# Optimization experiments

Hardware: AMD Instinct MI355X
Metric: run time of the kernel (lower is better)

The kernel has to match this reference:

```python
import jax, jax.numpy as jnp
import numpy as np

E, T, H, I, K = 16, 2048, 1024, 512, 2  # experts, tokens, hidden, intermediate, top_k


def setup_inputs() -> dict:
    key = jax.random.key(0)
    k1, k2, k3, k4, k5 = jax.random.split(key, 5)
    hidden_states = jax.random.normal(k1, (T, H), dtype=jnp.float32)
    topk_weights = jax.random.uniform(k2, (T, K), dtype=jnp.float32)
    topk_indices = jax.random.randint(k3, (T, K), 0, E, dtype=jnp.int32)
    # learned expert params, viewed per expert as in _view_experts_weight()
    gate_up_proj = jax.random.normal(k4, (E, H, 2 * I), dtype=jnp.float32) * 0.02
    down_proj = jax.random.normal(k5, (E, I, H), dtype=jnp.float32) * 0.02
    return {
        "hidden_states": hidden_states,
        "topk_weights": topk_weights,
        "topk_indices": topk_indices,
        "gate_up_proj": gate_up_proj,
        "down_proj": down_proj,
    }


def reference(hidden_states, topk_weights, topk_indices, gate_up_proj, down_proj):
    """MoE experts: per-expert gate_up GEMM -> silu-gate -> down GEMM,
    combined with top-k routing weights (index_add over tokens in the original).

    Equivalent dense formulation: combine[e, t] = sum_k topk_weights[t, k] * [topk_indices[t, k] == e];
    out = sum_e expert_e(hidden_states) * combine[e][:, None]. Tokens not routed to e get
    weight 0, matching the original gather/scatter-add exactly (including duplicate
    expert ids within a token, which accumulate).
    """
    num_experts = gate_up_proj.shape[0]
    one_hot = jax.nn.one_hot(topk_indices, num_experts, dtype=topk_weights.dtype)  # [T, K, E]
    combine = jnp.einsum("tk,tke->et", topk_weights, one_hot)  # [E, T]

    def body(acc, xs):
        w_gu, w_d, w = xs  # [H, 2I], [I, H], [T]
        gate_up = hidden_states @ w_gu  # [T, 2I]
        gate, up = jnp.split(gate_up, 2, axis=-1)
        expert_out = (jax.nn.silu(gate) * up) @ w_d  # [T, H]
        return acc + expert_out * w[:, None], None

    init = jnp.zeros_like(hidden_states)
    out, _ = jax.lax.scan(body, init, (gate_up_proj, down_proj, combine))
    return out.astype(hidden_states.dtype)
```

## Files before the change

kernel.cpp:

```cpp
#include <hip/hip_runtime.h>

#define E_ 16
#define T_ 2048
#define H_ 1024
#define I_ 512
#define NPAIR 4096
#define BM 128
#define MAXTILE 48

typedef __bf16 bf16x8 __attribute__((ext_vector_type(8)));
typedef float  f32x4  __attribute__((ext_vector_type(4)));

static __device__ __forceinline__ unsigned short f2bf(float f) {
    __bf16 h = (__bf16)f;
    return __builtin_bit_cast(unsigned short, h);
}

static __device__ __forceinline__ uint4 pack8(const float* v) {
    union { unsigned short us[8]; uint4 u; } r;
    #pragma unroll
    for (int i = 0; i < 8; ++i) r.us[i] = f2bf(v[i]);
    return r.u;
}

static __device__ __forceinline__ void gl_lds16(const void* g, void* l) {
    __builtin_amdgcn_global_load_lds(
        (const __attribute__((address_space(1))) unsigned int*)g,
        (__attribute__((address_space(3))) unsigned int*)l,
        16, 0, 0);
}

__global__ __launch_bounds__(256) void route_kernel(
    const float* __restrict__ tw, const int* __restrict__ ti,
    int* __restrict__ offs, int* __restrict__ tile_e, int* __restrict__ tile_r,
    int* __restrict__ pair_ts, float* __restrict__ pair_w)
{
    __shared__ unsigned short hist[256][E_];
    __shared__ int ebase[E_];
    const int tid = threadIdx.x;

    int e_loc[16];
    unsigned short h[E_];
    for (int e = 0; e < E_; ++e) h[e] = 0;
    for (int i = 0; i < 16; ++i) {
        int p = tid * 16 + i;
        int e = ti[p];
        e_loc[i] = e;
        h[e]++;
    }
    for (int e = 0; e < E_; ++e) hist[tid][e] = h[e];
    __syncthreads();

    if (tid < E_) {
        int e = tid, run = 0;
        for (int t = 0; t < 256; ++t) {
            unsigned short c = hist[t][e];
            hist[t][e] = (unsigned short)run;
            run += c;
        }
        ebase[e] = run;
    }
    __syncthreads();
    if (tid == 0) {
        int run = 0, nt = 0;
        for (int e = 0; e < E_; ++e) {
            int c = ebase[e];
            offs[e] = run; ebase[e] = run;
            for (int r = 0; r < c; r += BM) { tile_e[nt] = e; tile_r[nt] = r; ++nt; }
            run += c;
        }
        offs[E_] = run;
        for (; nt < MAXTILE; ++nt) tile_e[nt] = -1;
    }
    __syncthreads();

    int cur[E_];
    for (int e = 0; e < E_; ++e) cur[e] = ebase[e] + hist[tid][e];
    for (int i = 0; i < 16; ++i) {
        int p = tid * 16 + i;
        int e = e_loc[i];
        int pos = cur[e]++;
        pair_ts[pos] = p;
        pair_w[pos]  = tw[p];
    }
}

__global__ __launch_bounds__(256) void gather_kernel(
    const float* __restrict__ X, const int* __restrict__ pair_ts,
    unsigned short* __restrict__ Ag)
{
    const int q = blockIdx.x;
    const int t = pair_ts[q] >> 1;
    const int c = threadIdx.x * 4;
    const float4 x = *(const float4*)&X[(size_t)t * H_ + c];
    ushort4 b; b.x = f2bf(x.x); b.y = f2bf(x.y); b.z = f2bf(x.z); b.w = f2bf(x.w);
    *(ushort4*)&Ag[(size_t)q * H_ + c] = b;
}

#define MFMA_TILE(AS, BS)                                                              \
    _Pragma("unroll")                                                                  \
    for (int kkj = 0; kkj < 2; ++kkj) {                                                \
        const int j0 = kkj * 4;                                                        \
        bf16x8 af[4], bfr[2];                                                          \
        _Pragma("unroll")                                                              \
        for (int m = 0; m < 4; ++m)                                                    \
            af[m] = *(const bf16x8*)&AS[wm * 64 + m * 16 + lrow][((j0 + lk) ^ (lrow & 7)) * 8]; \
        _Pragma("unroll")                                                              \
        for (int n = 0; n < 2; ++n)                                                    \
            bfr[n] = *(const bf16x8*)&BS[wn * 32 + n * 16 + lrow][((j0 + lk) ^ (lrow & 7)) * 8]; \
        _Pragma("unroll")                                                              \
        for (int m = 0; m < 4; ++m)                                                    \
            _Pragma("unroll")                                                          \
            for (int n = 0; n < 2; ++n)                                                \
                acc[m][n] = __builtin_amdgcn_mfma_f32_16x16x32_bf16(af[m], bfr[n], acc[m][n], 0, 0, 0); \
    }

#define PIPE_STEP(KT, NT, BSTRIDE, ASC, ASN, BSC, BSN, BVC, BVN)                       \
    {                                                                                  \
        if ((KT) + 1 < (NT)) {                                                         \
            const int kb_ = ((KT) + 1) * 64;                                           \
            _Pragma("unroll")                                                          \
            for (int i = 0; i < 4; ++i) gl_lds16(asrc[i] + kb_, &ASN[w * 32 + i * 8][0]); \
            *(uint4*)&BSN[bn][bg0] = pack8(&BVC[0]);                                   \
            *(uint4*)&BSN[bn][bg1] = pack8(&BVC[8]);                                   \
        }                                                                              \
        if ((KT) + 2 < (NT)) {                                                         \
            const int kb2_ = ((KT) + 2) * 64;                                          \
            _Pragma("unroll")                                                          \
            for (int i = 0; i < 16; ++i)                                               \
                BVN[i] = bsrc[(size_t)(kb2_ + w * 16 + i) * (BSTRIDE)];                \
        }                                                                              \
        MFMA_TILE(ASC, BSC)                                                            \
        __syncthreads();                                                               \
    }

__global__ __launch_bounds__(256, 3) void gemm1_kernel(
    const unsigned short* __restrict__ Ag, const float* __restrict__ W1,
    const int* __restrict__ offs, const int* __restrict__ tile_e,
    const int* __restrict__ tile_r, unsigned short* __restrict__ act)
{
    const int e = tile_e[blockIdx.y];
    if (e < 0) return;
    const int rbeg = offs[e], rend = offs[e + 1];
    const int ne   = rend - rbeg;
    const int row0 = tile_r[blockIdx.y];
    const int c0 = blockIdx.x * 32;

    __shared__ unsigned short As0[128][64], As1[128][64];
    __shared__ unsigned short Bs0[64][64],  Bs1[64][64];

    const int tid  = threadIdx.x;
    const int lane = tid & 63;
    const int w    = tid >> 6;
    const int wm   = w >> 1, wn = w & 1;
    const int lrow = lane & 15;
    const int lk   = lane >> 4;

    const float* __restrict__ W1e = W1 + (size_t)e * (H_ * 2 * I_);

    const int r8 = lane >> 3, gr = lane & 7;
    const unsigned short* asrc[4];
    #pragma unroll
    for (int i = 0; i < 4; ++i) {
        int q = rbeg + row0 + w * 32 + i * 8 + r8;
        if (q > rend - 1) q = rend - 1;
        asrc[i] = Ag + (size_t)q * H_ + (gr ^ r8) * 8;
    }

    const int bn   = lane;
    const int bcol = ((bn >> 4) & 1) * I_ + c0 + (bn >> 5) * 16 + (bn & 15);
    const float* __restrict__ bsrc = W1e + bcol;
    const int bg0 = ((2 * w)     ^ (bn & 7)) * 8;
    const int bg1 = ((2 * w + 1) ^ (bn & 7)) * 8;

    f32x4 acc[4][2];
    #pragma unroll
    for (int m = 0; m < 4; ++m)
        #pragma unroll
        for (int n = 0; n < 2; ++n)
            acc[m][n] = f32x4{0.f, 0.f, 0.f, 0.f};

    float bv0[16], bv1[16];
    #pragma unroll
    for (int i = 0; i < 16; ++i) bv0[i] = bsrc[(size_t)(w * 16 + i) * (2 * I_)];
    #pragma unroll
    for (int i = 0; i < 16; ++i) bv1[i] = bsrc[(size_t)(64 + w * 16 + i) * (2 * I_)];
    #pragma unroll
    for (int i = 0; i < 4; ++i) gl_lds16(asrc[i], &As0[w * 32 + i * 8][0]);
    *(uint4*)&Bs0[bn][bg0] = pack8(&bv0[0]);
    *(uint4*)&Bs0[bn][bg1] = pack8(&bv0[8]);
    __syncthreads();

    for (int kt = 0; kt < 16; kt += 2) {
        PIPE_STEP(kt,     16, 2 * I_, As0, As1, Bs0, Bs1, bv1, bv0)
        PIPE_STEP(kt + 1, 16, 2 * I_, As1, As0, Bs1, Bs0, bv0, bv1)
    }

    for (int m = 0; m < 4; ++m) {
        #pragma unroll
        for (int reg = 0; reg < 4; ++reg) {
            int rloc = wm * 64 + m * 16 + lk * 4 + reg;
            if (row0 + rloc < ne) {
                int q = rbeg + row0 + rloc;
                float g = acc[m][0][reg], u = acc[m][1][reg];
                float a = g / (1.f + __expf(-g)) * u;
                act[(size_t)q * I_ + c0 + wn * 16 + lrow] = f2bf(a);
            }
        }
    }
}

__global__ __launch_bounds__(256, 3) void gemm2_kernel(
    const unsigned short* __restrict__ act, const float* __restrict__ W2,
    const int* __restrict__ offs, const int* __restrict__ tile_e,
    const int* __restrict__ tile_r, const int* __restrict__ pair_ts,
    const float* __restrict__ pair_w, float* __restrict__ out)
{
    const int e = tile_e[blockIdx.y];
    if (e < 0) return;
    const int rbeg = offs[e], rend = offs[e + 1];
    const int ne   = rend - rbeg;
    const int row0 = tile_r[blockIdx.y];
    const int c0 = blockIdx.x * 64;

    __shared__ unsigned short As0[128][64], As1[128][64];
    __shared__ unsigned short Bs0[64][64],  Bs1[64][64];

    const int tid  = threadIdx.x;
    const int lane = tid & 63;
    const int w    = tid >> 6;
    const int wm   = w >> 1, wn = w & 1;
    const int lrow = lane & 15;
    const int lk   = lane >> 4;

    const float* __restrict__ W2e = W2 + (size_t)e * (I_ * H_);

    const int r8 = lane >> 3, gr = lane & 7;
    const unsigned short* asrc[4];
    #pragma unroll
    for (int i = 0; i < 4; ++i) {
        int q = rbeg + row0 + w * 32 + i * 8 + r8;
        if (q > rend - 1) q = rend - 1;
        asrc[i] = act + (size_t)q * I_ + (gr ^ r8) * 8;
    }

    const int bn = lane;
    const float* __restrict__ bsrc = W2e + c0 + bn;
    const int bg0 = ((2 * w)     ^ (bn & 7)) * 8;
    const int bg1 = ((2 * w + 1) ^ (bn & 7)) * 8;

    f32x4 acc[4][2];
    #pragma unroll
    for (int m = 0; m < 4; ++m)
        #pragma unroll
        for (int n = 0; n < 2; ++n)
            acc[m][n] = f32x4{0.f, 0.f, 0.f, 0.f};

    float bv0[16], bv1[16];
    #pragma unroll
    for (int i = 0; i < 16; ++i) bv0[i] = bsrc[(size_t)(w * 16 + i) * H_];
    #pragma unroll
    for (int i = 0; i < 16; ++i) bv1[i] = bsrc[(size_t)(64 + w * 16 + i) * H_];
    #pragma unroll
    for (int i = 0; i < 4; ++i) gl_lds16(asrc[i], &As0[w * 32 + i * 8][0]);
    *(uint4*)&Bs0[bn][bg0] = pack8(&bv0[0]);
    *(uint4*)&Bs0[bn][bg1] = pack8(&bv0[8]);
    __syncthreads();

    for (int kt = 0; kt < 8; kt += 2) {
        PIPE_STEP(kt,     8, H_, As0, As1, Bs0, Bs1, bv1, bv0)
        PIPE_STEP(kt + 1, 8, H_, As1, As0, Bs1, Bs0, bv0, bv1)
    }

    for (int m = 0; m < 4; ++m) {
        #pragma unroll
        for (int reg = 0; reg < 4; ++reg) {
            int rloc = wm * 64 + m * 16 + lk * 4 + reg;
            if (row0 + rloc < ne) {
                int q   = rbeg + row0 + rloc;
                int t   = pair_ts[q] >> 1;
                float wt = pair_w[q];
                #pragma unroll
                for (int n = 0; n < 2; ++n) {
                    int cg = c0 + wn * 32 + n * 16 + lrow;
                    atomicAdd(&out[(size_t)t * H_ + cg], wt * acc[m][n][reg]);
                }
            }
        }
    }
}

extern "C" void kernel_launch(void* const* d_in, const int* in_sizes, int n_in,
                              void* d_out, int out_size, void* d_ws, size_t ws_size,
                              hipStream_t stream)
{
    const float* X  = (const float*)d_in[0];
    const float* tw = (const float*)d_in[1];
    const int*   ti = (const int*)d_in[2];
    const float* W1 = (const float*)d_in[3];
    const float* W2 = (const float*)d_in[4];
    float* out = (float*)d_out;

    char* ws = (char*)d_ws;
    int*   offs    = (int*)(ws);
    int*   tile_e  = (int*)(ws + 128);
    int*   tile_r  = (int*)(ws + 128 + MAXTILE * 4);
    int*   pair_ts = (int*)(ws + 1024);
    float* pair_w  = (float*)(ws + 1024 + NPAIR * 4);
    unsigned short* Ag  = (unsigned short*)(ws + (1u << 16));
    unsigned short* act = (unsigned short*)(ws + (1u << 16) + (size_t)NPAIR * H_ * 2);

    hipMemsetAsync(d_out, 0, (size_t)out_size * sizeof(float), stream);

    route_kernel<<<1, 256, 0, stream>>>(tw, ti, offs, tile_e, tile_r, pair_ts, pair_w);

    gather_kernel<<<NPAIR, 256, 0, stream>>>(X, pair_ts, Ag);

    gemm1_kernel<<<dim3(I_ / 32, MAXTILE), 256, 0, stream>>>(Ag, W1, offs, tile_e, tile_r, act);

    gemm2_kernel<<<dim3(H_ / 64, MAXTILE), 256, 0, stream>>>(act, W2, offs, tile_e, tile_r, pair_ts, pair_w, out);
}
```

Before: 80.21 us.

## Deepen K-loop pipeline with triple-buffered A tiles and manual waitcnt barriers

Replaces the double-buffered PIPE_STEP loop in both grouped GEMM kernels with a fully unrolled pipeline. It triple-buffers A tiles in LDS, keeps four rotating register buffers for the fp32 B prefetch, and issues loads two stages ahead. __syncthreads is replaced by explicit s_waitcnt vmcnt(20)/s_barrier so outstanding global loads can stay in flight across iterations, and MFMA sections are wrapped in s_setprio. The added LDS and register use lowers the launch_bounds occupancy hint from 3 to 2 blocks per CU, trading occupancy for deeper latency hiding. The hand-written vmcnt count is fragile if the compiler reorders or merges loads.

```diff
diff --git a/kernel.cpp b/kernel.cpp
--- a/kernel.cpp
+++ b/kernel.cpp
@@ -115,26 +115,57 @@
                 acc[m][n] = __builtin_amdgcn_mfma_f32_16x16x32_bf16(af[m], bfr[n], acc[m][n], 0, 0, 0); \
     }
 
-#define PIPE_STEP(KT, NT, BSTRIDE, ASC, ASN, BSC, BSN, BVC, BVN)                       \
-    {                                                                                  \
-        if ((KT) + 1 < (NT)) {                                                         \
-            const int kb_ = ((KT) + 1) * 64;                                           \
-            _Pragma("unroll")                                                          \
-            for (int i = 0; i < 4; ++i) gl_lds16(asrc[i] + kb_, &ASN[w * 32 + i * 8][0]); \
-            *(uint4*)&BSN[bn][bg0] = pack8(&BVC[0]);                                   \
-            *(uint4*)&BSN[bn][bg1] = pack8(&BVC[8]);                                   \
+#define ISSUE_BV(BV, KB, BSTRIDE)                                                      \
+    _Pragma("unroll")                                                                  \
+    for (int i = 0; i < 16; ++i)                                                       \
+        BV[i] = bsrc[(size_t)((KB) + w * 16 + i) * (BSTRIDE)];
+
+#define ISSUE_A(BUF, KB)                                                               \
+    _Pragma("unroll")                                                                  \
+    for (int i = 0; i < 4; ++i) gl_lds16(asrc[i] + (KB), &BUF[w * 32 + i * 8][0]);
+
+#define PACK_B(BS, BV)                                                                 \
+    *(uint4*)&BS[bn][bg0] = pack8(&(BV)[0]);                                           \
+    *(uint4*)&BS[bn][bg1] = pack8(&(BV)[8]);
+
+#define K_PIPELINE(NT, BSTRIDE)                                                        \
+    float bv0[16], bv1[16], bv2[16], bv3[16];                                          \
+    ISSUE_BV(bv0, 0, BSTRIDE)                                                          \
+    PACK_B(Bs[0], bv0)                                                                 \
+    ISSUE_A(As[0], 0)                                                                  \
+    __builtin_amdgcn_sched_barrier(0);                                                 \
+    ISSUE_BV(bv1, 64, BSTRIDE)                                                         \
+    ISSUE_A(As[1], 64)                                                                 \
+    asm volatile("s_waitcnt vmcnt(20) lgkmcnt(0)" ::: "memory");                       \
+    asm volatile("s_barrier" ::: "memory");                                            \
+    _Pragma("unroll")                                                                  \
+    for (int j = 0; j < (NT); ++j) {                                                   \
+        if (j + 2 < (NT)) {                                                            \
+            if (((j + 2) & 3) == 0) { ISSUE_BV(bv0, (j + 2) * 64, BSTRIDE) }           \
+            if (((j + 2) & 3) == 1) { ISSUE_BV(bv1, (j + 2) * 64, BSTRIDE) }           \
+            if (((j + 2) & 3) == 2) { ISSUE_BV(bv2, (j + 2) * 64, BSTRIDE) }           \
+            if (((j + 2) & 3) == 3) { ISSUE_BV(bv3, (j + 2) * 64, BSTRIDE) }           \
+            ISSUE_A(As[(j + 2) % 3], (j + 2) * 64)                                     \
         }                                                                              \
-        if ((KT) + 2 < (NT)) {                                                         \
-            const int kb2_ = ((KT) + 2) * 64;                                          \
-            _Pragma("unroll")                                                          \
-            for (int i = 0; i < 16; ++i)                                               \
-                BVN[i] = bsrc[(size_t)(kb2_ + w * 16 + i) * (BSTRIDE)];                \
+        if (j + 1 < (NT)) {                                                            \
+            if (((j + 1) & 3) == 0) { PACK_B(Bs[(j + 1) & 1], bv0) }                   \
+            if (((j + 1) & 3) == 1) { PACK_B(Bs[(j + 1) & 1], bv1) }                   \
+            if (((j + 1) & 3) == 2) { PACK_B(Bs[(j + 1) & 1], bv2) }                   \
+            if (((j + 1) & 3) == 3) { PACK_B(Bs[(j + 1) & 1], bv3) }                   \
         }                                                                              \
-        MFMA_TILE(ASC, BSC)                                                            \
-        __syncthreads();                                                               \
-    }
-
-__global__ __launch_bounds__(256, 3) void gemm1_kernel(
+        __builtin_amdgcn_s_setprio(1);                                                 \
+        MFMA_TILE(As[j % 3], Bs[j & 1])                                                \
+        __builtin_amdgcn_s_setprio(0);                                                 \
+        if (j + 2 < (NT)) {                                                            \
+            asm volatile("s_waitcnt vmcnt(20) lgkmcnt(0)" ::: "memory");               \
+            asm volatile("s_barrier" ::: "memory");                                    \
+        } else if (j + 1 < (NT)) {                                                     \
+            asm volatile("s_waitcnt vmcnt(0) lgkmcnt(0)" ::: "memory");                \
+            asm volatile("s_barrier" ::: "memory");                                    \
+        }                                                                              \
+    }
+
+__global__ __launch_bounds__(256, 2) void gemm1_kernel(
     const unsigned short* __restrict__ Ag, const float* __restrict__ W1,
     const int* __restrict__ offs, const int* __restrict__ tile_e,
     const int* __restrict__ tile_r, unsigned short* __restrict__ act)
@@ -146,8 +177,8 @@
     const int row0 = tile_r[blockIdx.y];
     const int c0 = blockIdx.x * 32;
 
-    __shared__ unsigned short As0[128][64], As1[128][64];
-    __shared__ unsigned short Bs0[64][64],  Bs1[64][64];
+    __shared__ unsigned short As[3][128][64];
+    __shared__ unsigned short Bs[2][64][64];
 
     const int tid  = threadIdx.x;
     const int lane = tid & 63;
@@ -180,21 +211,7 @@
         for (int n = 0; n < 2; ++n)
             acc[m][n] = f32x4{0.f, 0.f, 0.f, 0.f};
 
-    float bv0[16], bv1[16];
-    #pragma unroll
-    for (int i = 0; i < 16; ++i) bv0[i] = bsrc[(size_t)(w * 16 + i) * (2 * I_)];
-    #pragma unroll
-    for (int i = 0; i < 16; ++i) bv1[i] = bsrc[(size_t)(64 + w * 16 + i) * (2 * I_)];
-    #pragma unroll
-    for (int i = 0; i < 4; ++i) gl_lds16(asrc[i], &As0[w * 32 + i * 8][0]);
-    *(uint4*)&Bs0[bn][bg0] = pack8(&bv0[0]);
-    *(uint4*)&Bs0[bn][bg1] = pack8(&bv0[8]);
-    __syncthreads();
-
-    for (int kt = 0; kt < 16; kt += 2) {
-        PIPE_STEP(kt,     16, 2 * I_, As0, As1, Bs0, Bs1, bv1, bv0)
-        PIPE_STEP(kt + 1, 16, 2 * I_, As1, As0, Bs1, Bs0, bv0, bv1)
-    }
+    K_PIPELINE(16, 2 * I_)
 
     for (int m = 0; m < 4; ++m) {
         #pragma unroll
@@ -210,8 +227,8 @@
     }
 }
 
-__global__ __launch_bounds__(256, 3) void gemm2_kernel(
-    const unsigned short* __restrict__ act, const float* __restrict__ W2,
+__global__ __launch_bounds__(256, 2) void gemm2_kernel(
+    const unsigned short* __restrict__ actg, const float* __restrict__ W2,
     const int* __restrict__ offs, const int* __restrict__ tile_e,
     const int* __restrict__ tile_r, const int* __restrict__ pair_ts,
     const float* __restrict__ pair_w, float* __restrict__ out)
@@ -223,8 +240,8 @@
     const int row0 = tile_r[blockIdx.y];
     const int c0 = blockIdx.x * 64;
 
-    __shared__ unsigned short As0[128][64], As1[128][64];
-    __shared__ unsigned short Bs0[64][64],  Bs1[64][64];
+    __shared__ unsigned short As[3][128][64];
+    __shared__ unsigned short Bs[2][64][64];
 
     const int tid  = threadIdx.x;
     const int lane = tid & 63;
@@ -241,7 +258,7 @@
     for (int i = 0; i < 4; ++i) {
         int q = rbeg + row0 + w * 32 + i * 8 + r8;
         if (q > rend - 1) q = rend - 1;
-        asrc[i] = act + (size_t)q * I_ + (gr ^ r8) * 8;
+        asrc[i] = actg + (size_t)q * I_ + (gr ^ r8) * 8;
     }
 
     const int bn = lane;
@@ -256,21 +273,7 @@
         for (int n = 0; n < 2; ++n)
             acc[m][n] = f32x4{0.f, 0.f, 0.f, 0.f};
 
-    float bv0[16], bv1[16];
-    #pragma unroll
-    for (int i = 0; i < 16; ++i) bv0[i] = bsrc[(size_t)(w * 16 + i) * H_];
-    #pragma unroll
-    for (int i = 0; i < 16; ++i) bv1[i] = bsrc[(size_t)(64 + w * 16 + i) * H_];
-    #pragma unroll
-    for (int i = 0; i < 4; ++i) gl_lds16(asrc[i], &As0[w * 32 + i * 8][0]);
-    *(uint4*)&Bs0[bn][bg0] = pack8(&bv0[0]);
-    *(uint4*)&Bs0[bn][bg1] = pack8(&bv0[8]);
-    __syncthreads();
-
-    for (int kt = 0; kt < 8; kt += 2) {
-        PIPE_STEP(kt,     8, H_, As0, As1, Bs0, Bs1, bv1, bv0)
-        PIPE_STEP(kt + 1, 8, H_, As1, As0, Bs1, Bs0, bv0, bv1)
-    }
+    K_PIPELINE(8, H_)
 
     for (int m = 0; m < 4; ++m) {
         #pragma unroll
```

After: 96.97 us. +20.9%, slower.

## Pre-transform weights to swizzled bf16 tiles and load B directly into LDS

Applied to the files above, without the earlier changes.

Adds a transform kernel that converts the fp32 expert weights into bf16 tiles already transposed and XOR-swizzled into the LDS layout. The GEMM kernels then stage B with direct global-to-LDS copies instead of strided fp32 register loads followed by packing. This removes the conversion and strided access from the GEMM inner loop and adds scheduling priority around the MFMA block. In exchange it adds a full read and write pass over all weights on every call.

```diff
diff --git a/kernel.cpp b/kernel.cpp
--- a/kernel.cpp
+++ b/kernel.cpp
@@ -95,6 +95,67 @@
     const float4 x = *(const float4*)&X[(size_t)t * H_ + c];
     ushort4 b; b.x = f2bf(x.x); b.y = f2bf(x.y); b.z = f2bf(x.z); b.w = f2bf(x.w);
     *(ushort4*)&Ag[(size_t)q * H_ + c] = b;
+}
+
+__global__ __launch_bounds__(256) void transform_kernel(
+    const float* __restrict__ W1, const float* __restrict__ W2,
+    unsigned short* __restrict__ W1t, unsigned short* __restrict__ W2t)
+{
+    __shared__ float tile[64][65];
+    const int t   = threadIdx.x;
+    const int bid = blockIdx.x;
+
+    if (bid < 4096) {
+        const int cb = bid & 15, ks = (bid >> 4) & 15, e = bid >> 8;
+        const float* __restrict__ W1e = W1 + (size_t)e * (H_ * 2 * I_);
+        #pragma unroll
+        for (int i = 0; i < 4; ++i) {
+            int fi = i * 256 + t;
+            int row = fi >> 4, c4 = fi & 15;
+            const float* s = (c4 < 8)
+                ? (W1e + (size_t)(ks * 64 + row) * (2 * I_) + cb * 32 + c4 * 4)
+                : (W1e + (size_t)(ks * 64 + row) * (2 * I_) + I_ + cb * 32 + (c4 - 8) * 4);
+            *(float4*)&tile[row][c4 * 4] = *(const float4*)s;
+        }
+        __syncthreads();
+        unsigned short* __restrict__ dst =
+            W1t + ((size_t)(e * 16 + cb) * 16 + ks) * 4096;
+        #pragma unroll
+        for (int s2 = 0; s2 < 2; ++s2) {
+            int gidx = t * 2 + s2;
+            int bn = gidx >> 3, p = gidx & 7;
+            int kl = (p ^ (bn & 7)) * 8;
+            int c  = ((bn >> 4) & 1) * 32 + (bn >> 5) * 16 + (bn & 15);
+            float v[8];
+            #pragma unroll
+            for (int j = 0; j < 8; ++j) v[j] = tile[kl + j][c];
+            *(uint4*)&dst[(size_t)gidx * 8] = pack8(v);
+        }
+    } else {
+        const int b2 = bid - 4096;
+        const int hb = b2 & 15, ks = (b2 >> 4) & 7, e = b2 >> 7;
+        const float* __restrict__ W2e = W2 + (size_t)e * (I_ * H_);
+        #pragma unroll
+        for (int i = 0; i < 4; ++i) {
+            int fi = i * 256 + t;
+            int row = fi >> 4, c4 = fi & 15;
+            *(float4*)&tile[row][c4 * 4] =
+                *(const float4*)(W2e + (size_t)(ks * 64 + row) * H_ + hb * 64 + c4 * 4);
+        }
+        __syncthreads();
+        unsigned short* __restrict__ dst =
+            W2t + ((size_t)(e * 16 + hb) * 8 + ks) * 4096;
+        #pragma unroll
+        for (int s2 = 0; s2 < 2; ++s2) {
+            int gidx = t * 2 + s2;
+            int bn = gidx >> 3, p = gidx & 7;
+            int kl = (p ^ (bn & 7)) * 8;
+            float v[8];
+            #pragma unroll
+            for (int j = 0; j < 8; ++j) v[j] = tile[kl + j][bn];
+            *(uint4*)&dst[(size_t)gidx * 8] = pack8(v);
+        }
+    }
 }
 
 #define MFMA_TILE(AS, BS)                                                              \
@@ -115,27 +176,34 @@
                 acc[m][n] = __builtin_amdgcn_mfma_f32_16x16x32_bf16(af[m], bfr[n], acc[m][n], 0, 0, 0); \
     }
 
-#define PIPE_STEP(KT, NT, BSTRIDE, ASC, ASN, BSC, BSN, BVC, BVN)                       \
-    {                                                                                  \
-        if ((KT) + 1 < (NT)) {                                                         \
-            const int kb_ = ((KT) + 1) * 64;                                           \
-            _Pragma("unroll")                                                          \
-            for (int i = 0; i < 4; ++i) gl_lds16(asrc[i] + kb_, &ASN[w * 32 + i * 8][0]); \
-            *(uint4*)&BSN[bn][bg0] = pack8(&BVC[0]);                                   \
-            *(uint4*)&BSN[bn][bg1] = pack8(&BVC[8]);                                   \
-        }                                                                              \
-        if ((KT) + 2 < (NT)) {                                                         \
-            const int kb2_ = ((KT) + 2) * 64;                                          \
-            _Pragma("unroll")                                                          \
-            for (int i = 0; i < 16; ++i)                                               \
-                BVN[i] = bsrc[(size_t)(kb2_ + w * 16 + i) * (BSTRIDE)];                \
-        }                                                                              \
-        MFMA_TILE(ASC, BSC)                                                            \
+#define STAGE_A(BUF, KB)                                                               \
+    _Pragma("unroll")                                                                  \
+    for (int i = 0; i < 4; ++i) gl_lds16(asrc[i] + (KB), &As[BUF][w * 32 + i * 8][0]);
+
+#define STAGE_B(BUF, KS)                                                               \
+    _Pragma("unroll")                                                                  \
+    for (int i = 0; i < 2; ++i)                                                        \
+        gl_lds16(bsrcB + (size_t)(KS) * 4096 + i * 512,                                \
+                 &Bs[BUF][0][0] + w * 1024 + i * 512);
+
+#define K_PIPE(NT)                                                                     \
+    STAGE_A(0, 0)                                                                      \
+    STAGE_B(0, 0)                                                                      \
+    __syncthreads();                                                                   \
+    int cur = 0;                                                                       \
+    _Pragma("unroll")                                                                  \
+    for (int kt = 0; kt < (NT); ++kt) {                                                \
+        int nxt = cur ^ 1;                                                             \
+        if (kt + 1 < (NT)) { STAGE_A(nxt, (kt + 1) * 64) STAGE_B(nxt, kt + 1) }        \
+        __builtin_amdgcn_s_setprio(1);                                                 \
+        MFMA_TILE(As[cur], Bs[cur])                                                    \
+        __builtin_amdgcn_s_setprio(0);                                                 \
         __syncthreads();                                                               \
+        cur = nxt;                                                                     \
     }
 
 __global__ __launch_bounds__(256, 3) void gemm1_kernel(
-    const unsigned short* __restrict__ Ag, const float* __restrict__ W1,
+    const unsigned short* __restrict__ Ag, const unsigned short* __restrict__ W1t,
     const int* __restrict__ offs, const int* __restrict__ tile_e,
     const int* __restrict__ tile_r, unsigned short* __restrict__ act)
 {
@@ -144,10 +212,11 @@
     const int rbeg = offs[e], rend = offs[e + 1];
     const int ne   = rend - rbeg;
     const int row0 = tile_r[blockIdx.y];
-    const int c0 = blockIdx.x * 32;
-
-    __shared__ unsigned short As0[128][64], As1[128][64];
-    __shared__ unsigned short Bs0[64][64],  Bs1[64][64];
+    const int cb   = blockIdx.x;
+    const int c0   = cb * 32;
+
+    __shared__ unsigned short As[2][128][64];
+    __shared__ unsigned short Bs[2][64][64];
 
     const int tid  = threadIdx.x;
     const int lane = tid & 63;
@@ -156,8 +225,6 @@
     const int lrow = lane & 15;
     const int lk   = lane >> 4;
 
-    const float* __restrict__ W1e = W1 + (size_t)e * (H_ * 2 * I_);
-
     const int r8 = lane >> 3, gr = lane & 7;
     const unsigned short* asrc[4];
     #pragma unroll
@@ -167,11 +234,8 @@
         asrc[i] = Ag + (size_t)q * H_ + (gr ^ r8) * 8;
     }
 
-    const int bn   = lane;
-    const int bcol = ((bn >> 4) & 1) * I_ + c0 + (bn >> 5) * 16 + (bn & 15);
-    const float* __restrict__ bsrc = W1e + bcol;
-    const int bg0 = ((2 * w)     ^ (bn & 7)) * 8;
-    const int bg1 = ((2 * w + 1) ^ (bn & 7)) * 8;
+    const unsigned short* bsrcB =
+        W1t + ((size_t)(e * 16 + cb) * 16) * 4096 + w * 1024 + lane * 8;
 
     f32x4 acc[4][2];
     #pragma unroll
@@ -180,21 +244,7 @@
         for (int n = 0; n < 2; ++n)
             acc[m][n] = f32x4{0.f, 0.f, 0.f, 0.f};
 
-    float bv0[16], bv1[16];
-    #pragma unroll
-    for (int i = 0; i < 16; ++i) bv0[i] = bsrc[(size_t)(w * 16 + i) * (2 * I_)];
-    #pragma unroll
-    for (int i = 0; i < 16; ++i) bv1[i] = bsrc[(size_t)(64 + w * 16 + i) * (2 * I_)];
-    #pragma unroll
-    for (int i = 0; i < 4; ++i) gl_lds16(asrc[i], &As0[w * 32 + i * 8][0]);
-    *(uint4*)&Bs0[bn][bg0] = pack8(&bv0[0]);
-    *(uint4*)&Bs0[bn][bg1] = pack8(&bv0[8]);
-    __syncthreads();
-
-    for (int kt = 0; kt < 16; kt += 2) {
-        PIPE_STEP(kt,     16, 2 * I_, As0, As1, Bs0, Bs1, bv1, bv0)
-        PIPE_STEP(kt + 1, 16, 2 * I_, As1, As0, Bs1, Bs0, bv0, bv1)
-    }
+    K_PIPE(16)
 
     for (int m = 0; m < 4; ++m) {
         #pragma unroll
@@ -211,7 +261,7 @@
 }
 
 __global__ __launch_bounds__(256, 3) void gemm2_kernel(
-    const unsigned short* __restrict__ act, const float* __restrict__ W2,
+    const unsigned short* __restrict__ Agact, const unsigned short* __restrict__ W2t,
     const int* __restrict__ offs, const int* __restrict__ tile_e,
     const int* __restrict__ tile_r, const int* __restrict__ pair_ts,
     const float* __restrict__ pair_w, float* __restrict__ out)
@@ -221,10 +271,11 @@
     const int rbeg = offs[e], rend = offs[e + 1];
     const int ne   = rend - rbeg;
     const int row0 = tile_r[blockIdx.y];
-    const int c0 = blockIdx.x * 64;
-
-    __shared__ unsigned short As0[128][64], As1[128][64];
-    __shared__ unsigned short Bs0[64][64],  Bs1[64][64];
+    const int hb   = blockIdx.x;
+    const int c0   = hb * 64;
+
+    __shared__ unsigned short As[2][128][64];
+    __shared__ unsigned short Bs[2][64][64];
 
     const int tid  = threadIdx.x;
     const int lane = tid & 63;
@@ -233,21 +284,17 @@
     const int lrow = lane & 15;
     const int lk   = lane >> 4;
 
-    const float* __restrict__ W2e = W2 + (size_t)e * (I_ * H_);
-
     const int r8 = lane >> 3, gr = lane & 7;
     const unsigned short* asrc[4];
     #pragma unroll
     for (int i = 0; i < 4; ++i) {
         int q = rbeg + row0 + w * 32 + i * 8 + r8;
         if (q > rend - 1) q = rend - 1;
-        asrc[i] = act + (size_t)q * I_ + (gr ^ r8) * 8;
-    }
-
-    const int bn = lane;
-    const float* __restrict__ bsrc = W2e + c0 + bn;
-    const int bg0 = ((2 * w)     ^ (bn & 7)) * 8;
-    const int bg1 = ((2 * w + 1) ^ (bn & 7)) * 8;
+        asrc[i] = Agact + (size_t)q * I_ + (gr ^ r8) * 8;
+    }
+
+    const unsigned short* bsrcB =
+        W2t + ((size_t)(e * 16 + hb) * 8) * 4096 + w * 1024 + lane * 8;
 
     f32x4 acc[4][2];
     #pragma unroll
@@ -256,21 +303,7 @@
         for (int n = 0; n < 2; ++n)
             acc[m][n] = f32x4{0.f, 0.f, 0.f, 0.f};
 
-    float bv0[16], bv1[16];
-    #pragma unroll
-    for (int i = 0; i < 16; ++i) bv0[i] = bsrc[(size_t)(w * 16 + i) * H_];
-    #pragma unroll
-    for (int i = 0; i < 16; ++i) bv1[i] = bsrc[(size_t)(64 + w * 16 + i) * H_];
-    #pragma unroll
-    for (int i = 0; i < 4; ++i) gl_lds16(asrc[i], &As0[w * 32 + i * 8][0]);
-    *(uint4*)&Bs0[bn][bg0] = pack8(&bv0[0]);
-    *(uint4*)&Bs0[bn][bg1] = pack8(&bv0[8]);
-    __syncthreads();
-
-    for (int kt = 0; kt < 8; kt += 2) {
-        PIPE_STEP(kt,     8, H_, As0, As1, Bs0, Bs1, bv1, bv0)
-        PIPE_STEP(kt + 1, 8, H_, As1, As0, Bs1, Bs0, bv0, bv1)
-    }
+    K_PIPE(8)
 
     for (int m = 0; m < 4; ++m) {
         #pragma unroll
@@ -304,11 +337,13 @@
     char* ws = (char*)d_ws;
     int*   offs    = (int*)(ws);
     int*   tile_e  = (int*)(ws + 128);
-    int*   tile_r  = (int*)(ws + 128 + MAXTILE * 4);
+    int*   tile_r  = (int*)(ws + 320);
     int*   pair_ts = (int*)(ws + 1024);
     float* pair_w  = (float*)(ws + 1024 + NPAIR * 4);
-    unsigned short* Ag  = (unsigned short*)(ws + (1u << 16));
-    unsigned short* act = (unsigned short*)(ws + (1u << 16) + (size_t)NPAIR * H_ * 2);
+    unsigned short* Ag  = (unsigned short*)(ws + (size_t)(1u << 16));
+    unsigned short* act = (unsigned short*)(ws + (size_t)(1u << 16) + 8388608);
+    unsigned short* W1t = (unsigned short*)(ws + (size_t)(1u << 16) + 12582912);
+    unsigned short* W2t = (unsigned short*)(ws + (size_t)(1u << 16) + 46137344);
 
     hipMemsetAsync(d_out, 0, (size_t)out_size * sizeof(float), stream);
 
@@ -316,7 +351,9 @@
 
     gather_kernel<<<NPAIR, 256, 0, stream>>>(X, pair_ts, Ag);
 
-    gemm1_kernel<<<dim3(I_ / 32, MAXTILE), 256, 0, stream>>>(Ag, W1, offs, tile_e, tile_r, act);
-
-    gemm2_kernel<<<dim3(H_ / 64, MAXTILE), 256, 0, stream>>>(act, W2, offs, tile_e, tile_r, pair_ts, pair_w, out);
-}
+    transform_kernel<<<6144, 256, 0, stream>>>(W1, W2, W1t, W2t);
+
+    gemm1_kernel<<<dim3(16, MAXTILE), 256, 0, stream>>>(Ag, W1t, offs, tile_e, tile_r, act);
+
+    gemm2_kernel<<<dim3(16, MAXTILE), 256, 0, stream>>>(act, W2t, offs, tile_e, tile_r, pair_ts, pair_w, out);
+}
```

Result: slower. 93.48 us (+16.5%).
